# Kernel optimization log

Measured on AMD Instinct MI355X. Metric: run time of the kernel, lower is better.

The kernel has to match this reference:

```python
import jax, jax.numpy as jnp
import numpy as np

E = 1024   # embed_dim
H = 16     # num_heads
D = E // H # head_dim = 64
P = 32     # project_dim
BS = 32768


def setup_inputs() -> dict:
    key0 = jax.random.key(0)
    ks = jax.random.split(key0, 16)
    s = 0.02
    inp = {
        "query": jax.random.normal(ks[0], (BS, E), jnp.float32),
        "key": jax.random.normal(ks[1], (BS, E), jnp.float32),
        "value": jax.random.normal(ks[2], (BS, E), jnp.float32),
        "attn_bias": jax.random.normal(ks[3], (BS, H), jnp.float32),
        # q/k/v embedding linears: [E, H*D]
        "Wq": jax.random.normal(ks[4], (E, H * D), jnp.float32) * s,
        "bq": jnp.zeros((H * D,), jnp.float32),
        "Wk": jax.random.normal(ks[5], (E, H * D), jnp.float32) * s,
        "bk": jnp.zeros((H * D,), jnp.float32),
        "Wv": jax.random.normal(ks[6], (E, H * D), jnp.float32) * s,
        "bv": jnp.zeros((H * D,), jnp.float32),
        # key/value low-rank projection linears: [E, H*P]
        "We": jax.random.normal(ks[7], (E, H * P), jnp.float32) * s,
        "be": jnp.zeros((H * P,), jnp.float32),
        "Wf": jax.random.normal(ks[8], (E, H * P), jnp.float32) * s,
        "bf": jnp.zeros((H * P,), jnp.float32),
        # feature_expand: [H, H*P]
        "Wfe": jax.random.normal(ks[9], (H, H * P), jnp.float32) * s,
        "bfe": jnp.zeros((H * P,), jnp.float32),
        # out_linear: [H*D, E]
        "Wo": jax.random.normal(ks[10], (H * D, E), jnp.float32) * s,
        "bo": jnp.zeros((E,), jnp.float32),
    }
    return inp


def reference(query, key, value, attn_bias,
              Wq, bq, Wk, bk, Wv, bv,
              We, be, Wf, bf, Wfe, bfe, Wo, bo):
    bs = query.shape[0]
    scale = 1.0 / np.sqrt(D).astype(np.float32)

    q = (query @ Wq + bq).reshape(bs, H, D)   # [bs, H, D]
    k = (key @ Wk + bk).reshape(bs, H, D)     # [bs, H, D]
    v = (value @ Wv + bv).reshape(bs, H, D)   # [bs, H, D]
    e = (key @ We + be).reshape(bs, H, P)     # [bs, H, P]
    f = (value @ Wf + bf).reshape(bs, H, P)   # [bs, H, P]

    # With tgt_len=src_len=1: q @ (e @ k)^T == (q.k) * e  (outer-product collapse)
    qk = jnp.einsum('bhd,bhd->bh', q, k)                     # [bs, H]
    bias = (attn_bias @ Wfe + bfe).reshape(bs, H, P)          # [bs, H, P]
    attn = scale * qk[..., None] * e + bias                   # [bs, H, P]
    attn = jax.nn.softmax(attn, axis=-1)                      # dropout p=0 (eval)

    # attn @ (f @ v) == (attn.f) * v
    af = jnp.einsum('bhp,bhp->bh', attn, f)                   # [bs, H]
    out = (af[..., None] * v).reshape(bs, H * D) @ Wo + bo    # [bs, E]
    return out
```

## Files before the change

kernel.cpp:

```cpp
#include <hip/hip_runtime.h>
#include <hip/hip_bf16.h>
#include <stdint.h>

#define BS_N 32768
#define E_DIM 1024
#define H_N 16
#define HD 1024
#define HP 512

typedef __bf16 bf16x8 __attribute__((ext_vector_type(8)));
typedef float f32x4 __attribute__((ext_vector_type(4)));

__device__ __forceinline__ float asf(uint32_t u){ union{uint32_t u;float f;}x; x.u=u; return x.f; }
__device__ __forceinline__ uint32_t asu(float f){ union{float f;uint32_t u;}x; x.f=f; return x.u; }
__device__ __forceinline__ float blo(uint32_t u){ return asf(u<<16); }
__device__ __forceinline__ float bhi(uint32_t u){ return asf(u & 0xffff0000u); }
__device__ __forceinline__ uint16_t f2b(float f){
  uint32_t u = asu(f);
  u = u + 0x7fffu + ((u>>16)&1u);
  return (uint16_t)(u>>16);
}
__device__ __forceinline__ uint32_t pack2(float lo, float hi){
  return (uint32_t)f2b(lo) | ((uint32_t)f2b(hi)<<16);
}

#define GLD16(g, l) __builtin_amdgcn_global_load_lds( \
    (__attribute__((address_space(1))) const void*)(g), \
    (__attribute__((address_space(3))) void*)(l), 16, 0, 0)

__global__ __launch_bounds__(256) void cast_bf16(const float4* __restrict__ in,
                                                 uint2* __restrict__ out, int n4){
  int i = blockIdx.x*256 + threadIdx.x;
  int stride = gridDim.x*256;
  for (; i < n4; i += stride){
    float4 v = in[i];
    uint2 o; o.x = pack2(v.x, v.y); o.y = pack2(v.z, v.w);
    out[i] = o;
  }
}

__global__ __launch_bounds__(256) void transpose_cast(const float* __restrict__ W,
                                                      uint16_t* __restrict__ WT,
                                                      int R, int C){
  __shared__ float tile[32][33];
  int c0 = blockIdx.x*32, r0 = blockIdx.y*32;
  int tx = threadIdx.x, ty = threadIdx.y;
  #pragma unroll
  for (int i=0;i<32;i+=8) tile[ty+i][tx] = W[(size_t)(r0+ty+i)*C + c0+tx];
  __syncthreads();
  #pragma unroll
  for (int i=0;i<32;i+=8) WT[(size_t)(c0+ty+i)*R + r0+tx] = f2b(tile[tx][ty+i]);
}

__global__ __launch_bounds__(256) void prep_ab(const float* __restrict__ ab,
                                               uint16_t* __restrict__ abp){
  int i = blockIdx.x*256 + threadIdx.x;
  int b = i >> 5, j = i & 31;
  abp[i] = f2b(j < 16 ? ab[b*16 + j] : 0.f);
}

__global__ __launch_bounds__(256) void prep_wfe(const float* __restrict__ Wfe,
                                                uint16_t* __restrict__ WfeTp){
  int i = blockIdx.x*256 + threadIdx.x;
  int n = i >> 5, j = i & 31;
  float v = (j < 16) ? Wfe[j*512 + n] : 0.f;
  WfeTp[n*32 + j] = f2b(v);
}

template<int BF16OUT>
__global__ __launch_bounds__(256) void gemm_bt(const uint16_t* __restrict__ A,
                                               const uint16_t* __restrict__ BT,
                                               const float* __restrict__ bias,
                                               void* __restrict__ Cp,
                                               int N, int K){
  __shared__ alignas(16) uint16_t As[128*32];
  __shared__ alignas(16) uint16_t Bs[128*32];
  const int tid  = threadIdx.x;
  const int lane = tid & 63;
  const int w    = tid >> 6;
  const int wr   = w >> 1, wc = w & 1;

  int bid = (int)blockIdx.x;
  int nwg = (int)gridDim.x;
  int cpx = nwg >> 3;
  int swz = (bid & 7)*cpx + (bid >> 3);
  int rowTile = swz & 255;
  int colTile = swz >> 8;
  const size_t row0 = (size_t)rowTile << 7;
  const int col0 = colTile << 7;

  f32x4 acc[4][4];
  #pragma unroll
  for (int m=0;m<4;m++)
    #pragma unroll
    for (int n=0;n<4;n++){ f32x4 z = {0.f,0.f,0.f,0.f}; acc[m][n] = z; }

  const int c0 = tid, c1 = tid + 256;
  const int ar0 = c0 >> 2, ao0 = (c0 & 3) << 4;
  const int ar1 = c1 >> 2, ao1 = (c1 & 3) << 4;
  const size_t K2 = (size_t)K * 2;
  const char* Ab = (const char*)(A  + row0 * (size_t)K);
  const char* Bb = (const char*)(BT + (size_t)col0 * (size_t)K);
  const char* gA0 = Ab + (size_t)ar0*K2 + ao0;
  const char* gA1 = Ab + (size_t)ar1*K2 + ao1;
  const char* gB0 = Bb + (size_t)ar0*K2 + ao0;
  const char* gB1 = Bb + (size_t)ar1*K2 + ao1;
  char* lA0 = (char*)As + c0*16;
  char* lA1 = (char*)As + c1*16;
  char* lB0 = (char*)Bs + c0*16;
  char* lB1 = (char*)Bs + c1*16;

  const int r = lane & 15, kc = lane >> 4;
  const char* aRd = (const char*)As + ((wr<<6) + r)*64 + (kc<<4);
  const char* bRd = (const char*)Bs + ((wc<<6) + r)*64 + (kc<<4);

  for (int kt = 0; kt < K; kt += 32){
    GLD16(gA0 + kt*2, lA0);
    GLD16(gA1 + kt*2, lA1);
    GLD16(gB0 + kt*2, lB0);
    GLD16(gB1 + kt*2, lB1);
    __syncthreads();
    bf16x8 a[4], b[4];
    #pragma unroll
    for (int m=0;m<4;m++) a[m] = *(const bf16x8*)(aRd + m*1024);
    #pragma unroll
    for (int n=0;n<4;n++) b[n] = *(const bf16x8*)(bRd + n*1024);
    #pragma unroll
    for (int m=0;m<4;m++)
      #pragma unroll
      for (int n=0;n<4;n++)
        acc[m][n] = __builtin_amdgcn_mfma_f32_16x16x32_bf16(a[m], b[n], acc[m][n], 0, 0, 0);
    __syncthreads();
  }

  const int crow = (int)row0 + (wr<<6) + ((lane>>4)<<2);
  const int ccol = col0 + (wc<<6) + (lane & 15);
  #pragma unroll
  for (int n=0;n<4;n++){
    int col = ccol + n*16;
    float bv = bias[col];
    #pragma unroll
    for (int m=0;m<4;m++){
      #pragma unroll
      for (int j=0;j<4;j++){
        float val = acc[m][n][j] + bv;
        if (BF16OUT) ((uint16_t*)Cp)[(size_t)(crow + m*16 + j)*N + col] = f2b(val);
        else         ((float*)Cp)   [(size_t)(crow + m*16 + j)*N + col] = val;
      }
    }
  }
}

__global__ __launch_bounds__(256) void middle(const uint16_t* __restrict__ q,
                                              const uint16_t* __restrict__ k,
                                              const uint16_t* __restrict__ v,
                                              const uint16_t* __restrict__ e,
                                              const uint16_t* __restrict__ f,
                                              const uint16_t* __restrict__ bb,
                                              uint16_t* __restrict__ t){
  int tid = blockIdx.x*256 + threadIdx.x;
  int b = tid >> 4, h = tid & 15;
  size_t o64 = ((size_t)b << 10) + (h << 6);
  size_t o32 = ((size_t)b << 9)  + (h << 5);

  const uint4* qp = (const uint4*)(q + o64);
  const uint4* kp = (const uint4*)(k + o64);
  float qk = 0.f;
  #pragma unroll
  for (int i=0;i<8;i++){
    uint4 x = qp[i], y = kp[i];
    qk += blo(x.x)*blo(y.x) + bhi(x.x)*bhi(y.x);
    qk += blo(x.y)*blo(y.y) + bhi(x.y)*bhi(y.y);
    qk += blo(x.z)*blo(y.z) + bhi(x.z)*bhi(y.z);
    qk += blo(x.w)*blo(y.w) + bhi(x.w)*bhi(y.w);
  }
  qk *= 0.125f;

  const uint4* ep = (const uint4*)(e  + o32);
  const uint4* bp = (const uint4*)(bb + o32);
  float s[32];
  #pragma unroll
  for (int i=0;i<4;i++){
    uint4 ev = ep[i], bv = bp[i];
    s[i*8+0] = qk*blo(ev.x) + blo(bv.x);
    s[i*8+1] = qk*bhi(ev.x) + bhi(bv.x);
    s[i*8+2] = qk*blo(ev.y) + blo(bv.y);
    s[i*8+3] = qk*bhi(ev.y) + bhi(bv.y);
    s[i*8+4] = qk*blo(ev.z) + blo(bv.z);
    s[i*8+5] = qk*bhi(ev.z) + bhi(bv.z);
    s[i*8+6] = qk*blo(ev.w) + blo(bv.w);
    s[i*8+7] = qk*bhi(ev.w) + bhi(bv.w);
  }
  float mx = s[0];
  #pragma unroll
  for (int p=1;p<32;p++) mx = fmaxf(mx, s[p]);
  float sum = 0.f;
  #pragma unroll
  for (int p=0;p<32;p++){ s[p] = __expf(s[p]-mx); sum += s[p]; }

  const uint4* fp = (const uint4*)(f + o32);
  float af = 0.f;
  #pragma unroll
  for (int i=0;i<4;i++){
    uint4 fv = fp[i];
    af += s[i*8+0]*blo(fv.x) + s[i*8+1]*bhi(fv.x);
    af += s[i*8+2]*blo(fv.y) + s[i*8+3]*bhi(fv.y);
    af += s[i*8+4]*blo(fv.z) + s[i*8+5]*bhi(fv.z);
    af += s[i*8+6]*blo(fv.w) + s[i*8+7]*bhi(fv.w);
  }
  af /= sum;

  const uint4* vp = (const uint4*)(v + o64);
  uint4* tp = (uint4*)(t + o64);
  #pragma unroll
  for (int i=0;i<8;i++){
    uint4 vv = vp[i];
    uint4 o;
    o.x = pack2(af*blo(vv.x), af*bhi(vv.x));
    o.y = pack2(af*blo(vv.y), af*bhi(vv.y));
    o.z = pack2(af*blo(vv.z), af*bhi(vv.z));
    o.w = pack2(af*blo(vv.w), af*bhi(vv.w));
    tp[i] = o;
  }
}

extern "C" void kernel_launch(void* const* d_in, const int* in_sizes, int n_in,
                              void* d_out, int out_size, void* d_ws, size_t ws_size,
                              hipStream_t stream){
  const float* query = (const float*)d_in[0];
  const float* key   = (const float*)d_in[1];
  const float* value = (const float*)d_in[2];
  const float* ab    = (const float*)d_in[3];
  const float* Wq  = (const float*)d_in[4];
  const float* bq  = (const float*)d_in[5];
  const float* Wk  = (const float*)d_in[6];
  const float* bk  = (const float*)d_in[7];
  const float* Wv  = (const float*)d_in[8];
  const float* bv  = (const float*)d_in[9];
  const float* We  = (const float*)d_in[10];
  const float* be  = (const float*)d_in[11];
  const float* Wf  = (const float*)d_in[12];
  const float* bfp = (const float*)d_in[13];
  const float* Wfe = (const float*)d_in[14];
  const float* bfe = (const float*)d_in[15];
  const float* Wo  = (const float*)d_in[16];
  const float* bo  = (const float*)d_in[17];

  char* ws = (char*)d_ws;
  const size_t MB = (size_t)1 << 20;
  uint16_t* kb   = (uint16_t*)(ws +   0*MB);
  uint16_t* vb   = (uint16_t*)(ws +  64*MB);
  uint16_t* qb   = (uint16_t*)(ws + 128*MB);
  uint16_t* qo   = (uint16_t*)(ws + 192*MB);
  uint16_t* ko   = (uint16_t*)(ws + 256*MB);
  uint16_t* vo   = (uint16_t*)(ws + 320*MB);
  uint16_t* eo   = (uint16_t*)(ws + 384*MB);
  uint16_t* fo   = (uint16_t*)(ws + 416*MB);
  uint16_t* bb   = (uint16_t*)(ws + 448*MB);
  uint16_t* abp  = (uint16_t*)(ws + 480*MB);
  uint16_t* WqT  = (uint16_t*)(ws + 482*MB);
  uint16_t* WkT  = (uint16_t*)(ws + 484*MB);
  uint16_t* WvT  = (uint16_t*)(ws + 486*MB);
  uint16_t* WoT  = (uint16_t*)(ws + 488*MB);
  uint16_t* WeT  = (uint16_t*)(ws + 490*MB);
  uint16_t* WfT  = (uint16_t*)(ws + 491*MB);
  uint16_t* WfeTp= (uint16_t*)(ws + 492*MB);
  uint16_t* t    = qb;

  const int n4 = (BS_N*E_DIM)/4;
  cast_bf16<<<2048,256,0,stream>>>((const float4*)query, (uint2*)qb, n4);
  cast_bf16<<<2048,256,0,stream>>>((const float4*)key,   (uint2*)kb, n4);
  cast_bf16<<<2048,256,0,stream>>>((const float4*)value, (uint2*)vb, n4);

  dim3 tb(32,8);
  transpose_cast<<<dim3(32,32),tb,0,stream>>>(Wq, WqT, 1024, 1024);
  transpose_cast<<<dim3(32,32),tb,0,stream>>>(Wk, WkT, 1024, 1024);
  transpose_cast<<<dim3(32,32),tb,0,stream>>>(Wv, WvT, 1024, 1024);
  transpose_cast<<<dim3(32,32),tb,0,stream>>>(Wo, WoT, 1024, 1024);
  transpose_cast<<<dim3(16,32),tb,0,stream>>>(We, WeT, 1024, 512);
  transpose_cast<<<dim3(16,32),tb,0,stream>>>(Wf, WfT, 1024, 512);
  prep_ab<<<4096,256,0,stream>>>(ab, abp);
  prep_wfe<<<64,256,0,stream>>>(Wfe, WfeTp);

  gemm_bt<1><<<2048,256,0,stream>>>(qb,  WqT,   bq,  qo,   1024, 1024);
  gemm_bt<1><<<2048,256,0,stream>>>(kb,  WkT,   bk,  ko,   1024, 1024);
  gemm_bt<1><<<2048,256,0,stream>>>(vb,  WvT,   bv,  vo,   1024, 1024);
  gemm_bt<1><<<1024,256,0,stream>>>(kb,  WeT,   be,  eo,    512, 1024);
  gemm_bt<1><<<1024,256,0,stream>>>(vb,  WfT,   bfp, fo,    512, 1024);
  gemm_bt<1><<<1024,256,0,stream>>>(abp, WfeTp, bfe, bb,    512,   32);

  middle<<<2048,256,0,stream>>>(qo, ko, vo, eo, fo, bb, t);

  gemm_bt<0><<<2048,256,0,stream>>>(t, WoT, bo, d_out, 1024, 1024);
}
```

Before: 1.140 ms.

## Add 256x256 double-buffered MFMA GEMM and fuse K/E and V/F projections

Adds a new 512-thread GEMM kernel with 256x256 tiles, double-buffered LDS staging through global_load_lds, XOR-swizzled LDS reads, and interleaved MFMA/load phases with explicit waitcnts and barriers. The key and e projections, and likewise the value and f projections, are concatenated into single N=1536 GEMMs, so each activation input is streamed once instead of twice. The middle kernel is updated to read the concatenated outputs. The larger tiles raise register and LDS pressure, which lowers occupancy in exchange for more data reuse per tile.

```diff
diff --git a/kernel.cpp b/kernel.cpp
--- a/kernel.cpp
+++ b/kernel.cpp
@@ -4,9 +4,6 @@
 
 #define BS_N 32768
 #define E_DIM 1024
-#define H_N 16
-#define HD 1024
-#define HP 512
 
 typedef __bf16 bf16x8 __attribute__((ext_vector_type(8)));
 typedef float f32x4 __attribute__((ext_vector_type(4)));
@@ -28,6 +25,11 @@
     (__attribute__((address_space(1))) const void*)(g), \
     (__attribute__((address_space(3))) void*)(l), 16, 0, 0)
 
+#define BAR() __builtin_amdgcn_s_barrier()
+#define LGKM0() do{ asm volatile("s_waitcnt lgkmcnt(0)" ::: "memory"); __builtin_amdgcn_sched_barrier(0); }while(0)
+#define VMC4() do{ asm volatile("s_waitcnt vmcnt(4)" ::: "memory"); __builtin_amdgcn_sched_barrier(0); }while(0)
+#define VMC0() do{ asm volatile("s_waitcnt vmcnt(0)" ::: "memory"); __builtin_amdgcn_sched_barrier(0); }while(0)
+
 __global__ __launch_bounds__(256) void cast_bf16(const float4* __restrict__ in,
                                                  uint2* __restrict__ out, int n4){
   int i = blockIdx.x*256 + threadIdx.x;
@@ -65,6 +67,143 @@
   int n = i >> 5, j = i & 31;
   float v = (j < 16) ? Wfe[j*512 + n] : 0.f;
   WfeTp[n*32 + j] = f2b(v);
+}
+
+__global__ __launch_bounds__(256) void cat2(const float* __restrict__ a, int na,
+                                            const float* __restrict__ b, int nb,
+                                            float* __restrict__ o){
+  int i = blockIdx.x*256 + threadIdx.x;
+  if (i < na) o[i] = a[i];
+  else if (i < na + nb) o[i] = b[i - na];
+}
+
+template<int BF16OUT>
+__global__ __launch_bounds__(512, 2) void gemm256(const uint16_t* __restrict__ A,
+                                                  const uint16_t* __restrict__ BT,
+                                                  const float* __restrict__ bias,
+                                                  void* __restrict__ Cp,
+                                                  int N, int K){
+  __shared__ alignas(16) uint16_t As_[2][16384];
+  __shared__ alignas(16) uint16_t Bs_[2][16384];
+
+  const int tid  = threadIdx.x;
+  const int lane = tid & 63;
+  const int w    = tid >> 6;
+  const int wm   = w >> 2;
+  const int wn   = w & 3;
+  const int r    = lane & 15;
+  const int kc   = lane >> 4;
+
+  int bid = (int)blockIdx.x;
+  int nwg = (int)gridDim.x;
+  int cpx = nwg >> 3;
+  int swz = (bid & 7)*cpx + (bid >> 3);
+  const int rowTile = swz & 127;
+  const int colTile = swz >> 7;
+  const int row0 = rowTile << 8;
+  const int col0 = colTile << 8;
+
+  f32x4 acc[8][4];
+  #pragma unroll
+  for (int i=0;i<8;i++)
+    #pragma unroll
+    for (int j=0;j<4;j++){ f32x4 z = {0.f,0.f,0.f,0.f}; acc[i][j] = z; }
+
+  const int NT = K >> 6;
+  const size_t K2 = (size_t)K * 2;
+
+  const int sr  = tid >> 3;
+  const int scS = ((tid & 7) << 4) ^ ((sr & 7) << 4);
+  const char* gA = (const char*)(A  + (size_t)row0 * K) + (size_t)sr*K2 + scS;
+  const char* gB = (const char*)(BT + (size_t)col0 * K) + (size_t)sr*K2 + scS;
+  char* ldsA = (char*)&As_[0][0];
+  char* ldsB = (char*)&Bs_[0][0];
+
+  #define STAGE_A(b, hh, u) do{ \
+    const char* s_ = gA + (size_t)(hh)*(K2<<7) + ((size_t)(u)<<7); \
+    char* d_ = ldsA + ((b)<<15) + ((hh)<<14) + (tid<<4); \
+    GLD16(s_, d_); GLD16(s_ + (K2<<6), d_ + 8192); }while(0)
+  #define STAGE_B(b, hh, u) do{ \
+    const char* s_ = gB + (size_t)(hh)*(K2<<7) + ((size_t)(u)<<7); \
+    char* d_ = ldsB + ((b)<<15) + ((hh)<<14) + (tid<<4); \
+    GLD16(s_, d_); GLD16(s_ + (K2<<6), d_ + 8192); }while(0)
+
+  const int rdKey = (kc << 4) ^ ((r & 7) << 4);
+  const char* aR = ldsA + ((wm*128 + r) * 128);
+  const char* bR = ldsB + ((wn*64  + r) * 128);
+
+  bf16x8 afr[4][2], bf0[2][2], bf1[2][2];
+
+  #define READ_A(QM) do{ \
+    _Pragma("unroll") for (int fm=0; fm<4; ++fm) \
+    _Pragma("unroll") for (int ks=0; ks<2; ++ks) \
+      afr[fm][ks] = *(const bf16x8*)(aB + (QM)*8192 + fm*2048 + (rdKey ^ (ks<<6))); }while(0)
+  #define READ_B(DST, QN) do{ \
+    _Pragma("unroll") for (int fn=0; fn<2; ++fn) \
+    _Pragma("unroll") for (int ks=0; ks<2; ++ks) \
+      DST[fn][ks] = *(const bf16x8*)(bB + (QN)*4096 + fn*2048 + (rdKey ^ (ks<<6))); }while(0)
+  #define MFMA16(QM, QN, BF) do{ \
+    __builtin_amdgcn_s_setprio(1); \
+    _Pragma("unroll") for (int ks=0; ks<2; ++ks) \
+    _Pragma("unroll") for (int fm=0; fm<4; ++fm) \
+    _Pragma("unroll") for (int fn=0; fn<2; ++fn) \
+      acc[(QM)*4+fm][(QN)*2+fn] = __builtin_amdgcn_mfma_f32_16x16x32_bf16( \
+        afr[fm][ks], BF[fn][ks], acc[(QM)*4+fm][(QN)*2+fn], 0, 0, 0); \
+    __builtin_amdgcn_s_setprio(0); }while(0)
+
+  STAGE_B(0,0,0); STAGE_B(0,1,0); STAGE_A(0,0,0); STAGE_A(0,1,0);
+  if (NT > 1){ STAGE_B(1,0,1); STAGE_B(1,1,1); VMC4(); }
+  else       { VMC0(); }
+  BAR();
+
+  for (int t = 0; t < NT; ++t){
+    const int buf = t & 1;
+    const char* aB = aR + (buf << 15);
+    const char* bB = bR + (buf << 15);
+    READ_A(0); READ_B(bf0, 0);
+    if (t+1 < NT) STAGE_A(buf^1, 0, t+1);
+    BAR(); LGKM0();
+    MFMA16(0,0,bf0);
+    BAR();
+    READ_B(bf1, 1);
+    if (t+1 < NT) STAGE_A(buf^1, 1, t+1);
+    BAR(); LGKM0();
+    MFMA16(0,1,bf1);
+    BAR();
+    READ_A(1);
+    if (t+2 < NT) STAGE_B(buf, 0, t+2);
+    BAR(); LGKM0();
+    MFMA16(1,0,bf0);
+    BAR();
+    if (t+2 < NT) STAGE_B(buf, 1, t+2);
+    BAR(); LGKM0();
+    MFMA16(1,1,bf1);
+    if (t+2 < NT) { VMC4(); } else { VMC0(); }
+    BAR();
+  }
+
+  const int crow = row0 + wm*128 + ((lane>>4)<<2);
+  const int ccol = col0 + wn*64 + (lane & 15);
+  #pragma unroll
+  for (int i=0;i<8;i++){
+    #pragma unroll
+    for (int n=0;n<4;n++){
+      int col = ccol + n*16;
+      float bv = bias[col];
+      #pragma unroll
+      for (int j=0;j<4;j++){
+        float val = acc[i][n][j] + bv;
+        int row = crow + i*16 + j;
+        if (BF16OUT) ((uint16_t*)Cp)[(size_t)row*N + col] = f2b(val);
+        else         ((float*)Cp)   [(size_t)row*N + col] = val;
+      }
+    }
+  }
+  #undef STAGE_A
+  #undef STAGE_B
+  #undef READ_A
+  #undef READ_B
+  #undef MFMA16
 }
 
 template<int BF16OUT>
@@ -151,20 +290,16 @@
   }
 }
 
-__global__ __launch_bounds__(256) void middle(const uint16_t* __restrict__ q,
-                                              const uint16_t* __restrict__ k,
-                                              const uint16_t* __restrict__ v,
-                                              const uint16_t* __restrict__ e,
-                                              const uint16_t* __restrict__ f,
+__global__ __launch_bounds__(256) void middle(const uint16_t* __restrict__ qo,
+                                              const uint16_t* __restrict__ keo,
+                                              const uint16_t* __restrict__ vfo,
                                               const uint16_t* __restrict__ bb,
                                               uint16_t* __restrict__ t){
   int tid = blockIdx.x*256 + threadIdx.x;
   int b = tid >> 4, h = tid & 15;
-  size_t o64 = ((size_t)b << 10) + (h << 6);
-  size_t o32 = ((size_t)b << 9)  + (h << 5);
-
-  const uint4* qp = (const uint4*)(q + o64);
-  const uint4* kp = (const uint4*)(k + o64);
+
+  const uint4* qp = (const uint4*)(qo  + ((size_t)b<<10) + (h<<6));
+  const uint4* kp = (const uint4*)(keo + (size_t)b*1536 + (h<<6));
   float qk = 0.f;
   #pragma unroll
   for (int i=0;i<8;i++){
@@ -176,8 +311,8 @@
   }
   qk *= 0.125f;
 
-  const uint4* ep = (const uint4*)(e  + o32);
-  const uint4* bp = (const uint4*)(bb + o32);
+  const uint4* ep = (const uint4*)(keo + (size_t)b*1536 + 1024 + (h<<5));
+  const uint4* bp = (const uint4*)(bb  + ((size_t)b<<9) + (h<<5));
   float s[32];
   #pragma unroll
   for (int i=0;i<4;i++){
@@ -198,7 +333,7 @@
   #pragma unroll
   for (int p=0;p<32;p++){ s[p] = __expf(s[p]-mx); sum += s[p]; }
 
-  const uint4* fp = (const uint4*)(f + o32);
+  const uint4* fp = (const uint4*)(vfo + (size_t)b*1536 + 1024 + (h<<5));
   float af = 0.f;
   #pragma unroll
   for (int i=0;i<4;i++){
@@ -210,8 +345,8 @@
   }
   af /= sum;
 
-  const uint4* vp = (const uint4*)(v + o64);
-  uint4* tp = (uint4*)(t + o64);
+  const uint4* vp = (const uint4*)(vfo + (size_t)b*1536 + (h<<6));
+  uint4* tp = (uint4*)(t + ((size_t)b<<10) + (h<<6));
   #pragma unroll
   for (int i=0;i<8;i++){
     uint4 vv = vp[i];
@@ -248,24 +383,22 @@
 
   char* ws = (char*)d_ws;
   const size_t MB = (size_t)1 << 20;
-  uint16_t* kb   = (uint16_t*)(ws +   0*MB);
-  uint16_t* vb   = (uint16_t*)(ws +  64*MB);
-  uint16_t* qb   = (uint16_t*)(ws + 128*MB);
-  uint16_t* qo   = (uint16_t*)(ws + 192*MB);
-  uint16_t* ko   = (uint16_t*)(ws + 256*MB);
-  uint16_t* vo   = (uint16_t*)(ws + 320*MB);
-  uint16_t* eo   = (uint16_t*)(ws + 384*MB);
-  uint16_t* fo   = (uint16_t*)(ws + 416*MB);
-  uint16_t* bb   = (uint16_t*)(ws + 448*MB);
-  uint16_t* abp  = (uint16_t*)(ws + 480*MB);
-  uint16_t* WqT  = (uint16_t*)(ws + 482*MB);
-  uint16_t* WkT  = (uint16_t*)(ws + 484*MB);
-  uint16_t* WvT  = (uint16_t*)(ws + 486*MB);
-  uint16_t* WoT  = (uint16_t*)(ws + 488*MB);
-  uint16_t* WeT  = (uint16_t*)(ws + 490*MB);
-  uint16_t* WfT  = (uint16_t*)(ws + 491*MB);
-  uint16_t* WfeTp= (uint16_t*)(ws + 492*MB);
-  uint16_t* t    = qb;
+  uint16_t* kb    = (uint16_t*)(ws +   0*MB);
+  uint16_t* vb    = (uint16_t*)(ws +  64*MB);
+  uint16_t* qb    = (uint16_t*)(ws + 128*MB);
+  uint16_t* qo    = (uint16_t*)(ws + 192*MB);
+  uint16_t* keo   = (uint16_t*)(ws + 256*MB);
+  uint16_t* vfo   = (uint16_t*)(ws + 352*MB);
+  uint16_t* bb    = (uint16_t*)(ws + 448*MB);
+  uint16_t* abp   = (uint16_t*)(ws + 480*MB);
+  uint16_t* WqT   = (uint16_t*)(ws + 482*MB);
+  uint16_t* WkeT  = (uint16_t*)(ws + 484*MB);
+  uint16_t* WvfT  = (uint16_t*)(ws + 487*MB);
+  uint16_t* WoT   = (uint16_t*)(ws + 490*MB);
+  uint16_t* WfeTp = (uint16_t*)(ws + 492*MB);
+  float*    bke   = (float*)   (ws + 493*MB);
+  float*    bvf   = (float*)   (ws + 493*MB + 16384);
+  uint16_t* t     = qb;
 
   const int n4 = (BS_N*E_DIM)/4;
   cast_bf16<<<2048,256,0,stream>>>((const float4*)query, (uint2*)qb, n4);
@@ -274,22 +407,23 @@
 
   dim3 tb(32,8);
   transpose_cast<<<dim3(32,32),tb,0,stream>>>(Wq, WqT, 1024, 1024);
-  transpose_cast<<<dim3(32,32),tb,0,stream>>>(Wk, WkT, 1024, 1024);
-  transpose_cast<<<dim3(32,32),tb,0,stream>>>(Wv, WvT, 1024, 1024);
+  transpose_cast<<<dim3(32,32),tb,0,stream>>>(Wk, WkeT, 1024, 1024);
+  transpose_cast<<<dim3(16,32),tb,0,stream>>>(We, WkeT + (size_t)1024*1024, 1024, 512);
+  transpose_cast<<<dim3(32,32),tb,0,stream>>>(Wv, WvfT, 1024, 1024);
+  transpose_cast<<<dim3(16,32),tb,0,stream>>>(Wf, WvfT + (size_t)1024*1024, 1024, 512);
   transpose_cast<<<dim3(32,32),tb,0,stream>>>(Wo, WoT, 1024, 1024);
-  transpose_cast<<<dim3(16,32),tb,0,stream>>>(We, WeT, 1024, 512);
-  transpose_cast<<<dim3(16,32),tb,0,stream>>>(Wf, WfT, 1024, 512);
   prep_ab<<<4096,256,0,stream>>>(ab, abp);
   prep_wfe<<<64,256,0,stream>>>(Wfe, WfeTp);
-
-  gemm_bt<1><<<2048,256,0,stream>>>(qb,  WqT,   bq,  qo,   1024, 1024);
-  gemm_bt<1><<<2048,256,0,stream>>>(kb,  WkT,   bk,  ko,   1024, 1024);
-  gemm_bt<1><<<2048,256,0,stream>>>(vb,  WvT,   bv,  vo,   1024, 1024);
-  gemm_bt<1><<<1024,256,0,stream>>>(kb,  WeT,   be,  eo,    512, 1024);
-  gemm_bt<1><<<1024,256,0,stream>>>(vb,  WfT,   bfp, fo,    512, 1024);
-  gemm_bt<1><<<1024,256,0,stream>>>(abp, WfeTp, bfe, bb,    512,   32);
-
-  middle<<<2048,256,0,stream>>>(qo, ko, vo, eo, fo, bb, t);
-
-  gemm_bt<0><<<2048,256,0,stream>>>(t, WoT, bo, d_out, 1024, 1024);
-}
+  cat2<<<6,256,0,stream>>>(bk, 1024, be, 512, bke);
+  cat2<<<6,256,0,stream>>>(bv, 1024, bfp, 512, bvf);
+
+  gemm256<1><<<512,512,0,stream>>>(qb, WqT,  bq,  qo,  1024, 1024);
+  gemm256<1><<<768,512,0,stream>>>(kb, WkeT, bke, keo, 1536, 1024);
+  gemm256<1><<<768,512,0,stream>>>(vb, WvfT, bvf, vfo, 1536, 1024);
+
+  gemm_bt<1><<<1024,256,0,stream>>>(abp, WfeTp, bfe, bb, 512, 32);
+
+  middle<<<2048,256,0,stream>>>(qo, keo, vfo, bb, t);
+
+  gemm256<0><<<512,512,0,stream>>>(t, WoT, bo, d_out, 1024, 1024);
+}
```

Measured after the change: 972.0 us. 14.8% less time.
